# Optimization experiments

Measured on AMD Instinct MI355X. Metric: run time of the kernel, lower is better.

## Reference

```python
import jax, jax.numpy as jnp
import numpy as np

N_NODES = 2000
NEG_SLOPE = 0.01  # torch nn.LeakyReLU default


def setup_inputs() -> dict:
    key = jax.random.key(0)
    ks = jax.random.split(key, 7)
    B, T, N, F, E = 4, 12, N_NODES, 64, 32000
    state = jax.random.normal(ks[0], (B, T, N, F), dtype=jnp.float32)
    feature = jax.random.normal(ks[1], (N, F), dtype=jnp.float32)
    W = jax.random.normal(ks[2], (F, 2 * F), dtype=jnp.float32) / np.sqrt(2 * F)
    b = jnp.zeros((F,), dtype=jnp.float32)
    src = jax.random.randint(ks[3], (E,), 0, N)
    dst = jax.random.randint(ks[4], (E,), 0, N)
    dist = jax.random.uniform(ks[5], (E, 1), dtype=jnp.float32)
    return {"state": state, "feature": feature, "W": W, "b": b,
            "src": src, "dst": dst, "dist": dist}


def reference(state, feature, W, b, src, dst, dist):
    # state: [B,T,N,F] -> node-major [N,B,T,F] (matches unsqueeze/transpose/squeeze)
    s = jnp.moveaxis(state, 2, 0)                       # [N,B,T,F]
    s_src = s[src]                                      # [E,B,T,F] gather
    s_dst = s[dst]                                      # [E,B,T,F]
    h = jnp.concatenate([s_src, s_dst], axis=-1)        # [E,B,T,2F]
    alpha = jnp.einsum('ebtk,fk->ebtf', h, W) + b       # linear 2F->F
    alpha = jnp.where(alpha >= 0, alpha, NEG_SLOPE * alpha)  # LeakyReLU
    alpha = alpha * dist[:, None, None, :]              # dist [E,1] broadcast
    # segment softmax over incoming edges per destination node
    n = s.shape[0]
    m = jax.ops.segment_max(alpha, dst, num_segments=n)        # [N,B,T,F]
    ex = jnp.exp(alpha - m[dst])
    denom = jax.ops.segment_sum(ex, dst, num_segments=n)       # [N,B,T,F]
    w = ex / denom[dst]                                         # [E,B,T,F]
    new_state = jax.ops.segment_sum(w * s_src, dst, num_segments=n)
    new_state = jax.nn.relu(new_state)                  # [N,B,T,F]
    return jnp.moveaxis(new_state, 0, 2)                # [B,T,N,F]
```

## Files before the change

kernel.cpp:

```cpp
#include <hip/hip_runtime.h>
#include <hip/hip_bf16.h>
#include <hip/hip_fp16.h>
#include <math.h>


#define F_DIM 64
#define LOG2E 1.442695040888963f
#define DSTR 2048
#define RSTRIDE 128

typedef _Float16 f16x8 __attribute__((ext_vector_type(8)));
typedef float f32x4 __attribute__((ext_vector_type(4)));

__global__ __launch_bounds__(256) void gemm_hist(
    const float* __restrict__ state, const float* __restrict__ W,
    const float* __restrict__ bias,
    unsigned* __restrict__ PSh, __half* __restrict__ P2Bh,
    const int* __restrict__ dst, int* __restrict__ chunk_hist_T,
    int E, int N, int HB) {
    __shared__ int h[2048];
    int tid = threadIdx.x;
    if ((int)blockIdx.x < HB) {
        int c = blockIdx.x;
        for (int i = tid; i < N; i += 256) h[i] = 0;
        __syncthreads();
        int e = c * 256 + tid;
        if (e < E) atomicAdd(&h[dst[e]], 1);
        __syncthreads();
        for (int d = tid; d < N; d += 256)
            chunk_hist_T[c * DSTR + d] = h[d];
        return;
    }
    int gb = blockIdx.x - HB;
    int wv = tid >> 6, lane = tid & 63;
    int l15 = lane & 15, l4 = lane >> 4;

    f16x8 bf[8][2];
#pragma unroll
    for (int ct = 0; ct < 8; ++ct) {
        int j = ct * 16 + l15;
        const float* wp = (j < 64) ? (W + j * 128) : (W + (j - 64) * 128 + 64);
#pragma unroll
        for (int kh = 0; kh < 2; ++kh) {
            const float* p = wp + kh * 32 + l4 * 8;
            float4 w0 = *(const float4*)p;
            float4 w1 = *(const float4*)(p + 4);
            f16x8 hh;
            hh[0] = (_Float16)w0.x; hh[1] = (_Float16)w0.y;
            hh[2] = (_Float16)w0.z; hh[3] = (_Float16)w0.w;
            hh[4] = (_Float16)w1.x; hh[5] = (_Float16)w1.y;
            hh[6] = (_Float16)w1.z; hh[7] = (_Float16)w1.w;
            bf[ct][kh] = hh;
        }
    }
    float b0 = bias[l15], b1 = bias[16 + l15], b2 = bias[32 + l15], b3 = bias[48 + l15];

    int r = gb * 64 + wv * 16;

    const float* ap = state + (long)(r + l15) * 64 + l4 * 8;
    float4 a0 = *(const float4*)ap;
    float4 a1 = *(const float4*)(ap + 4);
    float4 a2 = *(const float4*)(ap + 32);
    float4 a3 = *(const float4*)(ap + 36);
    f16x8 af0, af1;
    af0[0] = (_Float16)a0.x; af0[1] = (_Float16)a0.y;
    af0[2] = (_Float16)a0.z; af0[3] = (_Float16)a0.w;
    af0[4] = (_Float16)a1.x; af0[5] = (_Float16)a1.y;
    af0[6] = (_Float16)a1.z; af0[7] = (_Float16)a1.w;
    af1[0] = (_Float16)a2.x; af1[1] = (_Float16)a2.y;
    af1[2] = (_Float16)a2.z; af1[3] = (_Float16)a2.w;
    af1[4] = (_Float16)a3.x; af1[5] = (_Float16)a3.y;
    af1[6] = (_Float16)a3.z; af1[7] = (_Float16)a3.w;

    f32x4 zero = {0.f, 0.f, 0.f, 0.f};
    f32x4 acc[8];
#pragma unroll
    for (int ct = 0; ct < 8; ++ct) {
        acc[ct] = __builtin_amdgcn_mfma_f32_16x16x32_f16(af0, bf[ct][0], zero, 0, 0, 0);
        acc[ct] = __builtin_amdgcn_mfma_f32_16x16x32_f16(af1, bf[ct][1], acc[ct], 0, 0, 0);
    }

    float bb0[4] = {b0, b1, b2, b3};
#pragma unroll
    for (int reg = 0; reg < 4; ++reg) {
        long rr = r + l4 * 4 + reg;
        const float* sp = state + rr * 64;
#pragma unroll
        for (int ct = 0; ct < 4; ++ct) {
            float sval = sp[ct * 16 + l15];
            __half2 hh = __floats2half2_rn(acc[ct][reg], sval);
            PSh[rr * 64 + ct * 16 + l15] = *(unsigned*)&hh;
        }
#pragma unroll
        for (int ct = 4; ct < 8; ++ct) {
            P2Bh[rr * 64 + (ct - 4) * 16 + l15] =
                __float2half(acc[ct][reg] + bb0[ct - 4]);
        }
    }
}

__global__ void scatter_pad_kernel(const int* __restrict__ dst, const int* __restrict__ src,
                                   const float* __restrict__ dist,
                                   const int* __restrict__ chunk_hist_T,
                                   int* __restrict__ counts,
                                   int* __restrict__ esrc, float* __restrict__ edist,
                                   int E, int N, int C) {
    int c = blockIdx.x;
    int t = threadIdx.x;
    if (c < C) {
        __shared__ int sdst[256];
        int e = c * 256 + t;
        int d = (e < E) ? dst[e] : -1;
        sdst[t] = d;
        __syncthreads();
        if (e >= E) return;
        int rk = 0;
#pragma unroll 8
        for (int j = 0; j < 256; j++)
            rk += (j < t && sdst[j] == d) ? 1 : 0;
        int pre = 0;
        int c2 = 0;
        for (; c2 + 4 <= c; c2 += 4) {
            int p0 = chunk_hist_T[(c2 + 0) * DSTR + d];
            int p1 = chunk_hist_T[(c2 + 1) * DSTR + d];
            int p2 = chunk_hist_T[(c2 + 2) * DSTR + d];
            int p3 = chunk_hist_T[(c2 + 3) * DSTR + d];
            pre += p0 + p1 + p2 + p3;
        }
        for (; c2 < c; ++c2) pre += chunk_hist_T[c2 * DSTR + d];
        int off = pre + rk;
        if (off < RSTRIDE) {
            esrc[d * RSTRIDE + off] = src[e] << 8;
            edist[d * RSTRIDE + off] = dist[e] * LOG2E;
        }
    } else {
        int d = (c - C) * 256 + t;
        if (d >= N) return;
        int tot = 0;
        for (int c2 = 0; c2 < C; ++c2)
            tot += chunk_hist_T[c2 * DSTR + d];
        counts[d] = tot;
        int st = (tot < RSTRIDE) ? tot : RSTRIDE;
        int* er = esrc + d * RSTRIDE;
        float* dr = edist + d * RSTRIDE;
        for (int i = st; i < RSTRIDE; ++i) { er[i] = 0; dr[i] = 0.f; }
    }
}


#define ECOMP(U, D, P2V, DEN, NUM)                                        \
    {                                                                     \
        float x;                                                          \
        asm("v_fma_mix_f32 %0, %1, %2, %3 op_sel:[0,0,0] op_sel_hi:[1,0,0]" \
            : "=v"(x) : "v"(U), "v"(fone), "v"(P2V));                     \
        float y0 = x * (D);                                               \
        float y1 = 0.01f * y0;                                            \
        float y = fmaxf(y0, y1);                                          \
        float p = __builtin_amdgcn_exp2f(y);                              \
        DEN += p;                                                         \
        asm("v_fma_mix_f32 %0, %1, %2, %0 op_sel:[0,1,0] op_sel_hi:[0,1,0]" \
            : "+v"(NUM) : "v"(p), "v"(U));                                \
    }

#define G4E4(EP, DP, Q, P2V, D0, D1, M0, M1)                              \
    {                                                                     \
        int4   sq = (EP)[Q];                                              \
        float4 dq = (DP)[Q];                                              \
        unsigned q0 = *(const unsigned*)(PSb + sq.x + f4);                \
        unsigned q1 = *(const unsigned*)(PSb + sq.y + f4);                \
        unsigned q2 = *(const unsigned*)(PSb + sq.z + f4);                \
        unsigned q3 = *(const unsigned*)(PSb + sq.w + f4);                \
        ECOMP(q0, dq.x, P2V, D0, M0)                                      \
        ECOMP(q1, dq.y, P2V, D1, M1)                                      \
        ECOMP(q2, dq.z, P2V, D0, M0)                                      \
        ECOMP(q3, dq.w, P2V, D1, M1)                                      \
    }

__global__ __launch_bounds__(64, 8) void gat_kernel(
    const unsigned* __restrict__ PSh, const __half* __restrict__ P2Bh,
    const int* __restrict__ esrc, const float* __restrict__ edist,
    const int* __restrict__ counts,
    float* __restrict__ out, int N, int NBT) {
    int b = blockIdx.x;
    int xcd = b & 7, j = b >> 3;
    int pr = j / 6, sub = j % 6;
    int f = threadIdx.x & 63;
    int bt = xcd * 6 + sub;
    const char* PSb = (const char*)PSh + (size_t)bt * N * 256;
    int f4 = f << 2;
    int n0 = pr * 2;
    int cnt0 = counts[n0], cnt1 = counts[n0 + 1];
    const int4*   ep0 = (const int4*)(esrc + n0 * RSTRIDE);
    const float4* dp0 = (const float4*)(edist + n0 * RSTRIDE);
    const int4*   ep1 = ep0 + (RSTRIDE / 4);
    const float4* dp1 = dp0 + (RSTRIDE / 4);
    int ob0 = ((bt * N + n0) << 6) + f;
    float p2_0 = __half2float(P2Bh[ob0]);
    float p2_1 = __half2float(P2Bh[ob0 + 64]);
    unsigned z = *(const unsigned*)(PSb + f4);
    float zs = __half22float2(*(const __half2*)&z).y;
    float fone = 1.0f;
    int cm0 = (cnt0 > RSTRIDE) ? RSTRIDE : cnt0;
    int cm1 = (cnt1 > RSTRIDE) ? RSTRIDE : cnt1;
    int nq0 = (cm0 + 3) >> 2, nq1 = (cm1 + 3) >> 2;
    int nqmin = (nq0 < nq1) ? nq0 : nq1;
    float denA0 = 0.f, denA1 = 0.f, numA0 = 0.f, numA1 = 0.f;
    float denB0 = 0.f, denB1 = 0.f, numB0 = 0.f, numB1 = 0.f;
    for (int q = 0; q < nqmin; ++q) {
        int4   sa = ep0[q], sb = ep1[q];
        float4 da = dp0[q], db = dp1[q];
        unsigned a0 = *(const unsigned*)(PSb + sa.x + f4);
        unsigned b0 = *(const unsigned*)(PSb + sb.x + f4);
        unsigned a1 = *(const unsigned*)(PSb + sa.y + f4);
        unsigned b1 = *(const unsigned*)(PSb + sb.y + f4);
        unsigned a2 = *(const unsigned*)(PSb + sa.z + f4);
        unsigned b2 = *(const unsigned*)(PSb + sb.z + f4);
        unsigned a3 = *(const unsigned*)(PSb + sa.w + f4);
        unsigned b3 = *(const unsigned*)(PSb + sb.w + f4);
        ECOMP(a0, da.x, p2_0, denA0, numA0)
        ECOMP(b0, db.x, p2_1, denB0, numB0)
        ECOMP(a1, da.y, p2_0, denA1, numA1)
        ECOMP(b1, db.y, p2_1, denB1, numB1)
        ECOMP(a2, da.z, p2_0, denA0, numA0)
        ECOMP(b2, db.z, p2_1, denB0, numB0)
        ECOMP(a3, da.w, p2_0, denA1, numA1)
        ECOMP(b3, db.w, p2_1, denB1, numB1)
    }
    for (int q = nqmin; q < nq0; ++q)
        G4E4(ep0, dp0, q, p2_0, denA0, denA1, numA0, numA1)
    for (int q = nqmin; q < nq1; ++q)
        G4E4(ep1, dp1, q, p2_1, denB0, denB1, numB0, numB1)
    float npad0 = (float)((nq0 << 2) - cm0);
    float npad1 = (float)((nq1 << 2) - cm1);
    float o0 = (cnt0 > 0)
        ? fmaxf((numA0 + numA1 - npad0 * zs) / (denA0 + denA1 - npad0), 0.f) : 0.f;
    float o1 = (cnt1 > 0)
        ? fmaxf((numB0 + numB1 - npad1 * zs) / (denB0 + denB1 - npad1), 0.f) : 0.f;
    out[ob0] = o0;
    out[ob0 + 64] = o1;
}


extern "C" void kernel_launch(void* const* d_in, const int* in_sizes, int n_in,
                              void* d_out, int out_size, void* d_ws, size_t ws_size,
                              hipStream_t stream) {
    const float* state = (const float*)d_in[0];
    const float* W     = (const float*)d_in[2];
    const float* bias  = (const float*)d_in[3];
    const int*   src   = (const int*)d_in[4];
    const int*   dst   = (const int*)d_in[5];
    const float* dist  = (const float*)d_in[6];
    float* out = (float*)d_out;

    int N   = in_sizes[1] / F_DIM;
    int E   = in_sizes[4];
    int NBT = in_sizes[0] / (N * F_DIM);
    int C   = (E + 255) / 256;

    size_t pelems = (size_t)NBT * N * F_DIM;
    unsigned* PSh = (unsigned*)d_ws;
    __half* P2Bh = (__half*)(PSh + pelems);
    int* counts       = (int*)(P2Bh + pelems);
    int* chunk_hist_T = counts + 2048;
    int* esrc         = chunk_hist_T + 128 * DSTR;
    float* edist      = (float*)(esrc + 2048 * RSTRIDE);

    int total_rows = NBT * N;
    gemm_hist<<<C + total_rows / 64, 256, 0, stream>>>(state, W, bias, PSh, P2Bh,
                                                       dst, chunk_hist_T, E, N, C);
    scatter_pad_kernel<<<C + (N + 255) / 256, 256, 0, stream>>>(
        dst, src, dist, chunk_hist_T, counts, esrc, edist, E, N, C);

    gat_kernel<<<8 * 6 * (N / 2), 64, 0, stream>>>(PSh, P2Bh, esrc, edist, counts,
                                                   out, N, NBT);
}
```

Baseline: 97.32 us.

## Build per-destination edge lists with wave ballots instead of histogram plus scatter

Replaces the chunked histogram and the prefix-scan scatter kernel with a single CSR-building kernel. In it, each wavefront owns four destination nodes, scans the whole dst array, and uses ballot and popcount to assign stable slots. This drops the chunk_hist_T buffer and one dependent pass, and gemm_pre no longer carries histogram blocks. In exchange, every wave reads all E dst entries, about 500 waves times 32000 reads, which leans heavily on L2.

```diff
diff --git a/kernel.cpp b/kernel.cpp
--- a/kernel.cpp
+++ b/kernel.cpp
@@ -6,32 +6,74 @@
 
 #define F_DIM 64
 #define LOG2E 1.442695040888963f
-#define DSTR 2048
 #define RSTRIDE 128
 
 typedef _Float16 f16x8 __attribute__((ext_vector_type(8)));
 typedef float f32x4 __attribute__((ext_vector_type(4)));
 
-__global__ __launch_bounds__(256) void gemm_hist(
+__global__ __launch_bounds__(256) void csr_kernel(
+    const int* __restrict__ dst, const int* __restrict__ src,
+    const float* __restrict__ dist,
+    int* __restrict__ counts, int* __restrict__ esrc, float* __restrict__ edist,
+    int E, int N) {
+    int wv = threadIdx.x >> 6, lane = threadIdx.x & 63;
+    int d0 = (blockIdx.x * 4 + wv) * 4;
+    if (d0 >= N) return;
+    unsigned long long lmask = (1ull << lane) - 1ull;
+    int c0 = 0, c1 = 0, c2 = 0, c3 = 0;
+    int dv = (lane < E) ? dst[lane] : -1;
+    for (int i = 0; i < E; i += 64) {
+        int en = i + 64 + lane;
+        int dvn = (en < E) ? dst[en] : -1;
+        unsigned long long m0 = __ballot(dv == d0);
+        unsigned long long m1 = __ballot(dv == d0 + 1);
+        unsigned long long m2 = __ballot(dv == d0 + 2);
+        unsigned long long m3 = __ballot(dv == d0 + 3);
+        if (m0 | m1 | m2 | m3) {
+            int e = i + lane;
+            int hit = (dv >= d0) && (dv <= d0 + 3);
+            int sv = 0; float dw = 0.f;
+            if (hit) { sv = src[e] << 8; dw = dist[e] * LOG2E; }
+            if (dv == d0) {
+                int r = c0 + __popcll(m0 & lmask);
+                if (r < RSTRIDE) { esrc[d0 * RSTRIDE + r] = sv; edist[d0 * RSTRIDE + r] = dw; }
+            }
+            if (dv == d0 + 1) {
+                int r = c1 + __popcll(m1 & lmask);
+                if (r < RSTRIDE) { esrc[(d0 + 1) * RSTRIDE + r] = sv; edist[(d0 + 1) * RSTRIDE + r] = dw; }
+            }
+            if (dv == d0 + 2) {
+                int r = c2 + __popcll(m2 & lmask);
+                if (r < RSTRIDE) { esrc[(d0 + 2) * RSTRIDE + r] = sv; edist[(d0 + 2) * RSTRIDE + r] = dw; }
+            }
+            if (dv == d0 + 3) {
+                int r = c3 + __popcll(m3 & lmask);
+                if (r < RSTRIDE) { esrc[(d0 + 3) * RSTRIDE + r] = sv; edist[(d0 + 3) * RSTRIDE + r] = dw; }
+            }
+        }
+        c0 += __popcll(m0); c1 += __popcll(m1);
+        c2 += __popcll(m2); c3 += __popcll(m3);
+        dv = dvn;
+    }
+    if (lane == 0) {
+        counts[d0] = c0; counts[d0 + 1] = c1;
+        counts[d0 + 2] = c2; counts[d0 + 3] = c3;
+    }
+    int s0 = (c0 < RSTRIDE) ? c0 : RSTRIDE;
+    for (int i = s0 + lane; i < RSTRIDE; i += 64) { esrc[d0 * RSTRIDE + i] = 0; edist[d0 * RSTRIDE + i] = 0.f; }
+    int s1 = (c1 < RSTRIDE) ? c1 : RSTRIDE;
+    for (int i = s1 + lane; i < RSTRIDE; i += 64) { esrc[(d0 + 1) * RSTRIDE + i] = 0; edist[(d0 + 1) * RSTRIDE + i] = 0.f; }
+    int s2 = (c2 < RSTRIDE) ? c2 : RSTRIDE;
+    for (int i = s2 + lane; i < RSTRIDE; i += 64) { esrc[(d0 + 2) * RSTRIDE + i] = 0; edist[(d0 + 2) * RSTRIDE + i] = 0.f; }
+    int s3 = (c3 < RSTRIDE) ? c3 : RSTRIDE;
+    for (int i = s3 + lane; i < RSTRIDE; i += 64) { esrc[(d0 + 3) * RSTRIDE + i] = 0; edist[(d0 + 3) * RSTRIDE + i] = 0.f; }
+}
+
+__global__ __launch_bounds__(256) void gemm_pre(
     const float* __restrict__ state, const float* __restrict__ W,
     const float* __restrict__ bias,
-    unsigned* __restrict__ PSh, __half* __restrict__ P2Bh,
-    const int* __restrict__ dst, int* __restrict__ chunk_hist_T,
-    int E, int N, int HB) {
-    __shared__ int h[2048];
+    unsigned* __restrict__ PSh, __half* __restrict__ P2Bh) {
     int tid = threadIdx.x;
-    if ((int)blockIdx.x < HB) {
-        int c = blockIdx.x;
-        for (int i = tid; i < N; i += 256) h[i] = 0;
-        __syncthreads();
-        int e = c * 256 + tid;
-        if (e < E) atomicAdd(&h[dst[e]], 1);
-        __syncthreads();
-        for (int d = tid; d < N; d += 256)
-            chunk_hist_T[c * DSTR + d] = h[d];
-        return;
-    }
-    int gb = blockIdx.x - HB;
     int wv = tid >> 6, lane = tid & 63;
     int l15 = lane & 15, l4 = lane >> 4;
 
@@ -55,7 +97,7 @@
     }
     float b0 = bias[l15], b1 = bias[16 + l15], b2 = bias[32 + l15], b3 = bias[48 + l15];
 
-    int r = gb * 64 + wv * 16;
+    int r = blockIdx.x * 64 + wv * 16;
 
     const float* ap = state + (long)(r + l15) * 64 + l4 * 8;
     float4 a0 = *(const float4*)ap;
@@ -96,54 +138,6 @@
             P2Bh[rr * 64 + (ct - 4) * 16 + l15] =
                 __float2half(acc[ct][reg] + bb0[ct - 4]);
         }
-    }
-}
-
-__global__ void scatter_pad_kernel(const int* __restrict__ dst, const int* __restrict__ src,
-                                   const float* __restrict__ dist,
-                                   const int* __restrict__ chunk_hist_T,
-                                   int* __restrict__ counts,
-                                   int* __restrict__ esrc, float* __restrict__ edist,
-                                   int E, int N, int C) {
-    int c = blockIdx.x;
-    int t = threadIdx.x;
-    if (c < C) {
-        __shared__ int sdst[256];
-        int e = c * 256 + t;
-        int d = (e < E) ? dst[e] : -1;
-        sdst[t] = d;
-        __syncthreads();
-        if (e >= E) return;
-        int rk = 0;
-#pragma unroll 8
-        for (int j = 0; j < 256; j++)
-            rk += (j < t && sdst[j] == d) ? 1 : 0;
-        int pre = 0;
-        int c2 = 0;
-        for (; c2 + 4 <= c; c2 += 4) {
-            int p0 = chunk_hist_T[(c2 + 0) * DSTR + d];
-            int p1 = chunk_hist_T[(c2 + 1) * DSTR + d];
-            int p2 = chunk_hist_T[(c2 + 2) * DSTR + d];
-            int p3 = chunk_hist_T[(c2 + 3) * DSTR + d];
-            pre += p0 + p1 + p2 + p3;
-        }
-        for (; c2 < c; ++c2) pre += chunk_hist_T[c2 * DSTR + d];
-        int off = pre + rk;
-        if (off < RSTRIDE) {
-            esrc[d * RSTRIDE + off] = src[e] << 8;
-            edist[d * RSTRIDE + off] = dist[e] * LOG2E;
-        }
-    } else {
-        int d = (c - C) * 256 + t;
-        if (d >= N) return;
-        int tot = 0;
-        for (int c2 = 0; c2 < C; ++c2)
-            tot += chunk_hist_T[c2 * DSTR + d];
-        counts[d] = tot;
-        int st = (tot < RSTRIDE) ? tot : RSTRIDE;
-        int* er = esrc + d * RSTRIDE;
-        float* dr = edist + d * RSTRIDE;
-        for (int i = st; i < RSTRIDE; ++i) { er[i] = 0; dr[i] = 0.f; }
     }
 }
 
@@ -255,21 +249,19 @@
     int N   = in_sizes[1] / F_DIM;
     int E   = in_sizes[4];
     int NBT = in_sizes[0] / (N * F_DIM);
-    int C   = (E + 255) / 256;
 
     size_t pelems = (size_t)NBT * N * F_DIM;
     unsigned* PSh = (unsigned*)d_ws;
     __half* P2Bh = (__half*)(PSh + pelems);
-    int* counts       = (int*)(P2Bh + pelems);
-    int* chunk_hist_T = counts + 2048;
-    int* esrc         = chunk_hist_T + 128 * DSTR;
-    float* edist      = (float*)(esrc + 2048 * RSTRIDE);
+    int* counts   = (int*)(P2Bh + pelems);
+    int* esrc     = counts + 2048;
+    float* edist  = (float*)(esrc + 2048 * RSTRIDE);
+
+    csr_kernel<<<(N + 15) / 16, 256, 0, stream>>>(dst, src, dist, counts,
+                                                  esrc, edist, E, N);
 
     int total_rows = NBT * N;
-    gemm_hist<<<C + total_rows / 64, 256, 0, stream>>>(state, W, bias, PSh, P2Bh,
-                                                       dst, chunk_hist_T, E, N, C);
-    scatter_pad_kernel<<<C + (N + 255) / 256, 256, 0, stream>>>(
-        dst, src, dist, chunk_hist_T, counts, esrc, edist, E, N, C);
+    gemm_pre<<<total_rows / 64, 256, 0, stream>>>(state, W, bias, PSh, P2Bh);
 
     gat_kernel<<<8 * 6 * (N / 2), 64, 0, stream>>>(PSh, P2Bh, esrc, edist, counts,
                                                    out, N, NBT);
```

Result: slower. 224.0 us (+130.2%).
